# Performance work log

Measured on AMD Instinct MI355X. Metric: run time of the kernel, lower is better.

## Reference

```python
import jax, jax.numpy as jnp
import numpy as np

NUM_Q = 8      # num_quantizers
K = 1024       # codebook_size (num_tokens)
D = 512        # feature dim
B, T = 16, 2000
BETA = 0.25    # commitment weight


def setup_inputs() -> dict:
    key = jax.random.key(0)
    kx, kc = jax.random.split(key)
    x = jax.random.normal(kx, (B, T, D), dtype=jnp.float32)
    # learned codebooks, one per quantizer stage: [NUM_Q, K, D]
    codebooks = jax.random.normal(kc, (NUM_Q, K, D), dtype=jnp.float32)
    return {"x": x, "codebooks": codebooks}


def _vq_stage(residual, codebook):
    """Single VQ layer: nearest-codeword search + straight-through + commitment loss.
    residual: [B, T, D]; codebook: [K, D]."""
    sg = jax.lax.stop_gradient
    # squared L2 distances via ||r||^2 - 2 r.e + ||e||^2  -> [B, T, K]
    r2 = jnp.sum(residual * residual, axis=-1, keepdims=True)          # [B,T,1]
    e2 = jnp.sum(codebook * codebook, axis=-1)                          # [K]
    dots = jnp.einsum('btd,kd->btk', residual, codebook)                # [B,T,K]
    dist = r2 - 2.0 * dots + e2
    indices = jnp.argmin(dist, axis=-1)                                 # [B,T] int
    quantized = codebook[indices]                                       # [B,T,D] gather
    # commitment + codebook loss (VQ-VAE style)
    loss = (BETA * jnp.mean((sg(quantized) - residual) ** 2)
            + jnp.mean((quantized - sg(residual)) ** 2))
    # straight-through estimator
    quantized_st = residual + sg(quantized - residual)
    return quantized_st, indices, loss


def reference(x, codebooks):
    def step(carry, codebook):
        residual, q_out = carry
        q, idx, loss = _vq_stage(residual, codebook)
        residual = residual - jax.lax.stop_gradient(q)
        return (residual, q_out + q), (idx, loss)

    init = (x, jnp.zeros_like(x))
    (_, quantized_out), (all_indices, all_losses) = jax.lax.scan(step, init, codebooks)
    # all_indices: [NUM_Q, B, T]; mean loss across stages
    return quantized_out, all_indices, jnp.mean(all_losses)
```

## Files before the change

### kernel.cpp

```cpp
#include <hip/hip_runtime.h>

#define M_TOK 32000
#define DIM   512
#define KCB   1024
#define NQ    8
#define BM 256
#define NITER 24

typedef _Float16 f16x8 __attribute__((ext_vector_type(8)));
typedef _Float16 f16x4 __attribute__((ext_vector_type(4)));
typedef float f32x4 __attribute__((ext_vector_type(4)));

#define SBAR() __builtin_amdgcn_s_barrier()
#define SFENCE() __builtin_amdgcn_sched_barrier(0)
#define WAIT_VM(N) asm volatile("s_waitcnt vmcnt(" #N ")" ::: "memory")
#define WAIT_LGKM0() asm volatile("s_waitcnt lgkmcnt(0)" ::: "memory")

__device__ __forceinline__ void gload_lds16(const void* g, void* l) {
  __builtin_amdgcn_global_load_lds(
      (const __attribute__((address_space(1))) unsigned int*)g,
      (__attribute__((address_space(3))) unsigned int*)l, 16, 0, 0);
}

__device__ __forceinline__ float wave_reduce_sum(float v) {
#pragma unroll
  for (int off = 32; off > 0; off >>= 1) v += __shfl_xor(v, off, 64);
  return v;
}

__device__ __forceinline__ unsigned int fenc(float f) {
  unsigned int u = __float_as_uint(f);
  return (u & 0x80000000u) ? ~u : (u | 0x80000000u);
}

__device__ __forceinline__ _Float16 hi16(float v) { return (_Float16)v; }
__device__ __forceinline__ _Float16 lo16(float v, _Float16 h) {
  return (_Float16)(v - (float)h);
}

struct Split4 { f16x4 h, l; };
__device__ __forceinline__ Split4 split4(float4 v) {
  Split4 s;
  s.h[0] = hi16(v.x); s.l[0] = lo16(v.x, s.h[0]);
  s.h[1] = hi16(v.y); s.l[1] = lo16(v.y, s.h[1]);
  s.h[2] = hi16(v.z); s.l[2] = lo16(v.z, s.h[2]);
  s.h[3] = hi16(v.w); s.l[3] = lo16(v.w, s.h[3]);
  return s;
}

__global__ __launch_bounds__(256) void rvq_init_kernel(
    const float* __restrict__ x, const float* __restrict__ cb,
    float* __restrict__ e2, float* __restrict__ r2,
    unsigned long long* __restrict__ keys, float* __restrict__ lossCell,
    _Float16* __restrict__ ahi, _Float16* __restrict__ alo) {
  if (blockIdx.x == 0 && threadIdx.x == 0) *lossCell = 0.f;
  for (int i = blockIdx.x * 256 + threadIdx.x; i < M_TOK; i += gridDim.x * 256)
    keys[i] = ~0ull;
  int row = blockIdx.x * 4 + (threadIdx.x >> 6);
  int lane = threadIdx.x & 63;
  if (row < NQ * KCB) {
    const float4* s4 = (const float4*)(cb + (size_t)row * DIM);
    float s = 0.f;
    float4 v = s4[lane];
    s += v.x * v.x + v.y * v.y + v.z * v.z + v.w * v.w;
    v = s4[lane + 64];
    s += v.x * v.x + v.y * v.y + v.z * v.z + v.w * v.w;
    s = wave_reduce_sum(s);
    if (lane == 0) e2[row] = s;
  } else {
    int t = row - NQ * KCB;
    if (t >= M_TOK) return;
    const float4* s4 = (const float4*)(x + (size_t)t * DIM);
    float4 v0 = s4[lane], v1 = s4[lane + 64];
    float s = v0.x * v0.x + v0.y * v0.y + v0.z * v0.z + v0.w * v0.w
            + v1.x * v1.x + v1.y * v1.y + v1.z * v1.z + v1.w * v1.w;
    Split4 s0 = split4(v0), s1 = split4(v1);
    size_t base = (size_t)t * DIM + lane * 4;
    *(f16x4*)(ahi + base) = s0.h;
    *(f16x4*)(alo + base) = s0.l;
    *(f16x4*)(ahi + base + 256) = s1.h;
    *(f16x4*)(alo + base + 256) = s1.l;
    s = wave_reduce_sum(s);
    if (lane == 0) r2[t] = s;
  }
}

__global__ __launch_bounds__(256) void rvq_split_cb_kernel(
    const float* __restrict__ cb, _Float16* __restrict__ cbF) {
  int gid = blockIdx.x * 256 + threadIdx.x;
  int lane = gid & 63;
  int g = (gid >> 6) & 7;
  int half = (gid >> 9) & 1;
  int nc = (gid >> 10) & 3;
  int bt = (gid >> 12) & 31;
  int s = gid >> 17;
  if (s >= NQ) return;
  int col = nc * 256 + half * 128 + (g >> 2) * 64 + (g & 3) * 16 + (lane & 15);
  int ko = (bt & 15) * 32 + (lane >> 4) * 8;
  const float* src = cb + ((size_t)s * KCB + col) * DIM + ko;
  int isLo = bt >> 4;
  f16x8 out;
#pragma unroll
  for (int j = 0; j < 8; ++j) {
    _Float16 h = hi16(src[j]);
    out[j] = isLo ? lo16(src[j], h) : h;
  }
  *(f16x8*)(cbF + (size_t)gid * 8) = out;
}

__global__ __launch_bounds__(512, 2) void rvq_argmin_kernel(
    const _Float16* __restrict__ ahi,
    const _Float16* __restrict__ alo,
    const _Float16* __restrict__ cbFs,
    const float* __restrict__ e2,
    const float* __restrict__ r2,
    unsigned long long* __restrict__ keys) {
  __shared__ _Float16 bufA[2][2][2][4096];
  __shared__ _Float16 bufB[2][2][2][4096];

  const int tid = threadIdx.x;
  const int lane = tid & 63, w = tid >> 6;
  const int l15 = lane & 15, l4 = lane >> 4;
  const int wr = w >> 2, wc = w & 3;

  const int bid = blockIdx.x;
  const int xcd = bid & 7, org = bid >> 3;
  const int wg = ((xcd < 4) ? xcd * 63 : 252 + (xcd - 4) * 62) + org;
  const int m0 = (wg >> 2) * BM;
  const int nc = wg & 3;

  auto stage = [&](int nb, int tIter, int hp) {
    const int ktl = hp >> 2, half = hp & 1, isB = (hp >> 1) & 1;
    const int t = tIter * 2 + ktl;
    const int j = t & 15, p = t >> 4;
    if (!isB) {
      const _Float16* plane = (p == 2) ? alo : ahi;
      const int row = m0 + half * 128 + w * 16 + l15;
      const int ko = j * 32 + l4 * 8;
      gload_lds16(plane + (size_t)row * 512 + ko, &bufA[nb][ktl][half][w * 512]);
    } else {
      const int bt = (p == 1) ? 16 + j : j;
      const _Float16* base = cbFs + (((size_t)(bt * 4 + nc)) * 2 + half) * 4096;
      gload_lds16(base + tid * 8, &bufB[nb][ktl][half][w * 512]);
    }
  };

  f32x4 acc[8][4];
#pragma unroll
  for (int a = 0; a < 8; ++a)
#pragma unroll
    for (int b = 0; b < 4; ++b) acc[a][b] = (f32x4){0.f, 0.f, 0.f, 0.f};

#pragma unroll
  for (int hp = 0; hp < 8; ++hp) stage(0, 0, hp);
  WAIT_VM(4);
  SBAR();

  for (int it = 0; it < NITER; ++it) {
    const int pb = it & 1, nb = pb ^ 1;
    const int nt = (it + 1 == NITER) ? 0 : it + 1;
#pragma unroll
    for (int ph = 0; ph < 4; ++ph) {
      const int kt = ph >> 1, mfh = ph & 1;
      const _Float16* As = &bufA[pb][kt][wr][0];
      const _Float16* Bs = &bufB[pb][kt][wc >> 1][0];
      f16x8 af[4], bf[4];
#pragma unroll
      for (int i = 0; i < 4; ++i)
        af[i] = *(const f16x8*)(As + ((mfh * 4 + i) * 64 + lane) * 8);
#pragma unroll
      for (int i = 0; i < 4; ++i)
        bf[i] = *(const f16x8*)(Bs + (((wc & 1) * 4 + i) * 64 + lane) * 8);
      SFENCE();
      stage(nb, nt, 2 * ph);
      stage(nb, nt, 2 * ph + 1);
      if (ph == 1) WAIT_VM(4);
      if (ph == 3) WAIT_VM(4);
      SBAR();
      WAIT_LGKM0();
      SFENCE();
      __builtin_amdgcn_s_setprio(1);
#pragma unroll
      for (int j = 0; j < 4; ++j)
#pragma unroll
        for (int i = 0; i < 4; ++i)
          acc[mfh * 4 + i][j] = __builtin_amdgcn_mfma_f32_16x16x32_f16(
              af[i], bf[j], acc[mfh * 4 + i][j], 0, 0, 0);
      __builtin_amdgcn_s_setprio(0);
      SBAR();
    }
  }
  WAIT_VM(0);

  const int colbase = nc * 256 + (wc >> 1) * 128 + (wc & 1) * 64;
  float minv[32];
  int mini[32];
#pragma unroll
  for (int i = 0; i < 32; ++i) { minv[i] = 3.4e38f; mini[i] = 0; }
#pragma unroll
  for (int nf = 0; nf < 4; ++nf) {
    float e2v = e2[colbase + nf * 16 + l15];
    int colg = colbase + nf * 16 + l15;
#pragma unroll
    for (int mf = 0; mf < 8; ++mf) {
      float4 rv = *(const float4*)(r2 + m0 + wr * 128 + mf * 16 + l4 * 4);
      float rva[4] = {rv.x, rv.y, rv.z, rv.w};
#pragma unroll
      for (int rr = 0; rr < 4; ++rr) {
        float d = (rva[rr] - 2.f * acc[mf][nf][rr]) + e2v;
        int ii = mf * 4 + rr;
        if (d < minv[ii]) { minv[ii] = d; mini[ii] = colg; }
      }
    }
  }
#pragma unroll
  for (int mf = 0; mf < 8; ++mf) {
#pragma unroll
    for (int rr = 0; rr < 4; ++rr) {
      int ii = mf * 4 + rr;
      float v = minv[ii];
      int ix = mini[ii];
#pragma unroll
      for (int off = 8; off; off >>= 1) {
        float ov = __shfl_xor(v, off, 16);
        int oi = __shfl_xor(ix, off, 16);
        if (ov < v || (ov == v && oi < ix)) { v = ov; ix = oi; }
      }
      if (l15 == 0) {
        int tok = m0 + wr * 128 + mf * 16 + l4 * 4 + rr;
        unsigned long long key = ((unsigned long long)fenc(v) << 32) | (unsigned)ix;
        atomicMin(&keys[tok], key);
      }
    }
  }
}

__global__ __launch_bounds__(256) void rvq_update_kernel(
    const float* __restrict__ rin, const float* __restrict__ cb,
    unsigned long long* __restrict__ keys,
    float* __restrict__ rout, float* __restrict__ r2out,
    float* __restrict__ idx_out, float* __restrict__ lossCell,
    _Float16* __restrict__ ahi, _Float16* __restrict__ alo) {
  const int wave = threadIdx.x >> 6, lane = threadIdx.x & 63;
  __shared__ float lred[4];
  float lpart = 0.f;
  for (int r = wave; r < 64; r += 4) {
    const int tok = blockIdx.x * 64 + r;
    const unsigned idx = (unsigned)(keys[tok] & 0xffffffffu);
    const float4* rrow = (const float4*)(rin + (size_t)tok * DIM);
    const float4* crow = (const float4*)(cb + (size_t)idx * DIM);
    float4* orow = (float4*)(rout + (size_t)tok * DIM);
    float ssq_t = 0.f, ssq_r = 0.f;
#pragma unroll
    for (int c4 = 0; c4 < 2; ++c4) {
      int c = lane + c4 * 64;
      float4 a = rrow[c], q = crow[c];
      float4 t = make_float4(q.x - a.x, q.y - a.y, q.z - a.z, q.w - a.w);
      float4 qst = make_float4(a.x + t.x, a.y + t.y, a.z + t.z, a.w + t.w);
      float4 rn = make_float4(a.x - qst.x, a.y - qst.y, a.z - qst.z, a.w - qst.w);
      orow[c] = rn;
      Split4 sp = split4(rn);
      *(f16x4*)(ahi + (size_t)tok * DIM + c * 4) = sp.h;
      *(f16x4*)(alo + (size_t)tok * DIM + c * 4) = sp.l;
      ssq_t += t.x * t.x + t.y * t.y + t.z * t.z + t.w * t.w;
      ssq_r += rn.x * rn.x + rn.y * rn.y + rn.z * rn.z + rn.w * rn.w;
    }
    float tot_t = wave_reduce_sum(ssq_t);
    float tot_r = wave_reduce_sum(ssq_r);
    if (lane == 0) {
      idx_out[tok] = (float)idx;
      keys[tok] = ~0ull;
      r2out[tok] = tot_r;
      lpart += tot_t;
    }
  }
  if (lane == 0) lred[wave] = lpart;
  __syncthreads();
  if (threadIdx.x == 0)
    atomicAdd(lossCell, lred[0] + lred[1] + lred[2] + lred[3]);
}

__global__ __launch_bounds__(256) void rvq_finalize_kernel(
    const float* __restrict__ x, float* __restrict__ out,
    const float* __restrict__ lossCell, float* __restrict__ loss_out) {
  size_t i = (size_t)blockIdx.x * 256 + threadIdx.x;
  const size_t n4 = (size_t)M_TOK * DIM / 4;
  if (i < n4) {
    const float4* x4 = (const float4*)x;
    float4* o4 = (float4*)out;
    float4 a = x4[i], r = o4[i];
    o4[i] = make_float4(a.x - r.x, a.y - r.y, a.z - r.z, a.w - r.w);
  }
  if (blockIdx.x == 0 && threadIdx.x == 0) {
    *loss_out = *lossCell * (1.25f / 131072000.f);
  }
}

extern "C" void kernel_launch(void* const* d_in, const int* in_sizes, int n_in,
                              void* d_out, int out_size, void* d_ws, size_t ws_size,
                              hipStream_t stream) {
  const float* x = (const float*)d_in[0];
  const float* cb = (const float*)d_in[1];
  float* out = (float*)d_out;
  float* idx_out = out + (size_t)M_TOK * DIM;
  float* loss_out = idx_out + (size_t)NQ * M_TOK;

  char* wsp = (char*)d_ws;
  unsigned long long* keys = (unsigned long long*)wsp;
  float* e2 = (float*)(wsp + 262144);
  float* r2 = (float*)(wsp + 294912);
  float* lossCell = (float*)(wsp + 425984);
  _Float16* cbF = (_Float16*)(wsp + 524288);
  _Float16* ahi = (_Float16*)(wsp + 524288 + 16777216);
  _Float16* alo = ahi + (size_t)M_TOK * DIM;

  {
    int rows = NQ * KCB + M_TOK;
    rvq_init_kernel<<<(rows + 3) / 4, 256, 0, stream>>>(x, cb, e2, r2, keys,
                                                        lossCell, ahi, alo);
    rvq_split_cb_kernel<<<(NQ << 17) / 256, 256, 0, stream>>>(cb, cbF);
  }
  float* resbuf = out;
  const size_t stageF = (size_t)1 << 20;
  for (int s = 0; s < NQ; ++s) {
    const float* rin = (s == 0) ? x : resbuf;
    rvq_argmin_kernel<<<(M_TOK / BM) * 4, 512, 0, stream>>>(
        ahi, alo, cbF + (size_t)s * stageF, e2 + s * KCB, r2, keys);
    rvq_update_kernel<<<M_TOK / 64, 256, 0, stream>>>(
        rin, cb + (size_t)s * KCB * DIM, keys, resbuf, r2,
        idx_out + (size_t)s * M_TOK, lossCell, ahi, alo);
  }
  rvq_finalize_kernel<<<(M_TOK * DIM / 4 + 255) / 256, 256, 0, stream>>>(
      x, out, lossCell, loss_out);
}
```

Baseline: 1.297 ms.

## Switch argmin GEMM to triple-buffered LDS pipeline with one barrier per k-tile

Restructures the main argmin GEMM loop. The old double-buffered, four-phase-per-iteration schedule becomes a triple-buffered ring that prefetches two k-tiles ahead and uses a single barrier per tile. Each wave now loads all 8 A fragments and 4 B fragments per tile and issues 32 MFMAs between barriers, and the codebook pre-split layout is changed to match. LDS usage rises to about 96KB, so launch bounds drop to one block per CU. Fewer barriers and deeper prefetch are traded for lower occupancy.

```diff
diff --git a/kernel.cpp b/kernel.cpp
--- a/kernel.cpp
+++ b/kernel.cpp
@@ -5,7 +5,7 @@
 #define KCB   1024
 #define NQ    8
 #define BM 256
-#define NITER 24
+#define NT 48
 
 typedef _Float16 f16x8 __attribute__((ext_vector_type(8)));
 typedef _Float16 f16x4 __attribute__((ext_vector_type(4)));
@@ -14,7 +14,6 @@
 #define SBAR() __builtin_amdgcn_s_barrier()
 #define SFENCE() __builtin_amdgcn_sched_barrier(0)
 #define WAIT_VM(N) asm volatile("s_waitcnt vmcnt(" #N ")" ::: "memory")
-#define WAIT_LGKM0() asm volatile("s_waitcnt lgkmcnt(0)" ::: "memory")
 
 __device__ __forceinline__ void gload_lds16(const void* g, void* l) {
   __builtin_amdgcn_global_load_lds(
@@ -88,16 +87,14 @@
 __global__ __launch_bounds__(256) void rvq_split_cb_kernel(
     const float* __restrict__ cb, _Float16* __restrict__ cbF) {
   int gid = blockIdx.x * 256 + threadIdx.x;
-  int lane = gid & 63;
-  int g = (gid >> 6) & 7;
-  int half = (gid >> 9) & 1;
+  int c = gid & 1023;
   int nc = (gid >> 10) & 3;
   int bt = (gid >> 12) & 31;
   int s = gid >> 17;
   if (s >= NQ) return;
-  int col = nc * 256 + half * 128 + (g >> 2) * 64 + (g & 3) * 16 + (lane & 15);
-  int ko = (bt & 15) * 32 + (lane >> 4) * 8;
-  const float* src = cb + ((size_t)s * KCB + col) * DIM + ko;
+  int col = nc * 256 + (c >> 6) * 16 + (c & 15);
+  int k = (bt & 15) * 32 + ((c >> 4) & 3) * 8;
+  const float* src = cb + ((size_t)s * KCB + col) * DIM + k;
   int isLo = bt >> 4;
   f16x8 out;
 #pragma unroll
@@ -108,15 +105,15 @@
   *(f16x8*)(cbF + (size_t)gid * 8) = out;
 }
 
-__global__ __launch_bounds__(512, 2) void rvq_argmin_kernel(
+__global__ __launch_bounds__(512, 1) void rvq_argmin_kernel(
     const _Float16* __restrict__ ahi,
     const _Float16* __restrict__ alo,
-    const _Float16* __restrict__ cbFs,
+    const _Float16* __restrict__ cbF,
     const float* __restrict__ e2,
     const float* __restrict__ r2,
     unsigned long long* __restrict__ keys) {
-  __shared__ _Float16 bufA[2][2][2][4096];
-  __shared__ _Float16 bufB[2][2][2][4096];
+  __shared__ _Float16 bufA[3][8192];
+  __shared__ _Float16 bufB[3][8192];
 
   const int tid = threadIdx.x;
   const int lane = tid & 63, w = tid >> 6;
@@ -129,21 +126,23 @@
   const int m0 = (wg >> 2) * BM;
   const int nc = wg & 3;
 
-  auto stage = [&](int nb, int tIter, int hp) {
-    const int ktl = hp >> 2, half = hp & 1, isB = (hp >> 1) & 1;
-    const int t = tIter * 2 + ktl;
-    const int j = t & 15, p = t >> 4;
-    if (!isB) {
-      const _Float16* plane = (p == 2) ? alo : ahi;
-      const int row = m0 + half * 128 + w * 16 + l15;
-      const int ko = j * 32 + l4 * 8;
-      gload_lds16(plane + (size_t)row * 512 + ko, &bufA[nb][ktl][half][w * 512]);
-    } else {
-      const int bt = (p == 1) ? 16 + j : j;
-      const _Float16* base = cbFs + (((size_t)(bt * 4 + nc)) * 2 + half) * 4096;
-      gload_lds16(base + tid * 8, &bufB[nb][ktl][half][w * 512]);
-    }
+  const int c0 = tid, c1 = tid + 512;
+  const size_t aoff0 = (size_t)(m0 + (c0 >> 6) * 16 + (c0 & 15)) * DIM + ((c0 >> 4) & 3) * 8;
+  const size_t aoff1 = (size_t)(m0 + (c1 >> 6) * 16 + (c1 & 15)) * DIM + ((c1 >> 4) & 3) * 8;
+
+  auto stageB = [&](int t, _Float16* dst) {
+    int j = t & 15;
+    int bt = (t >= 16 && t < 32) ? 16 + j : j;
+    const _Float16* src = cbF + (size_t)(bt * 4 + nc) * 8192;
+    gload_lds16(src + (size_t)c0 * 8, dst + (size_t)c0 * 8);
+    gload_lds16(src + (size_t)c1 * 8, dst + (size_t)c1 * 8);
   };
+  auto stageA = [&](int t, _Float16* dst) {
+    const _Float16* plane = (t >= 32) ? alo : ahi;
+    const int ko = (t & 15) * 32;
+    gload_lds16(plane + aoff0 + ko, dst + (size_t)c0 * 8);
+    gload_lds16(plane + aoff1 + ko, dst + (size_t)c1 * 8);
+  };
 
   f32x4 acc[8][4];
 #pragma unroll
@@ -151,56 +150,54 @@
 #pragma unroll
     for (int b = 0; b < 4; ++b) acc[a][b] = (f32x4){0.f, 0.f, 0.f, 0.f};
 
-#pragma unroll
-  for (int hp = 0; hp < 8; ++hp) stage(0, 0, hp);
+  stageB(0, bufB[0]); stageA(0, bufA[0]);
+  stageB(1, bufB[1]); stageA(1, bufA[1]);
   WAIT_VM(4);
+  SFENCE();
   SBAR();
-
-  for (int it = 0; it < NITER; ++it) {
-    const int pb = it & 1, nb = pb ^ 1;
-    const int nt = (it + 1 == NITER) ? 0 : it + 1;
-#pragma unroll
-    for (int ph = 0; ph < 4; ++ph) {
-      const int kt = ph >> 1, mfh = ph & 1;
-      const _Float16* As = &bufA[pb][kt][wr][0];
-      const _Float16* Bs = &bufB[pb][kt][wc >> 1][0];
-      f16x8 af[4], bf[4];
-#pragma unroll
-      for (int i = 0; i < 4; ++i)
-        af[i] = *(const f16x8*)(As + ((mfh * 4 + i) * 64 + lane) * 8);
-#pragma unroll
-      for (int i = 0; i < 4; ++i)
-        bf[i] = *(const f16x8*)(Bs + (((wc & 1) * 4 + i) * 64 + lane) * 8);
-      SFENCE();
-      stage(nb, nt, 2 * ph);
-      stage(nb, nt, 2 * ph + 1);
-      if (ph == 1) WAIT_VM(4);
-      if (ph == 3) WAIT_VM(4);
-      SBAR();
-      WAIT_LGKM0();
+  SFENCE();
+
+  for (int it6 = 0; it6 < NT; it6 += 6) {
+#pragma unroll
+    for (int ph = 0; ph < 6; ++ph) {
+      const int t = it6 + ph;
+      const int rb = ph % 3;
+      const int wb = (ph + 2) % 3;
+      if (t < NT - 2) { stageB(t + 2, bufB[wb]); stageA(t + 2, bufA[wb]); }
+      const _Float16* As = bufA[rb];
+      const _Float16* Bs = bufB[rb];
+      f16x8 af[8], bf[4];
+#pragma unroll
+      for (int mf = 0; mf < 8; ++mf)
+        af[mf] = *(const f16x8*)(As + ((size_t)(wr * 8 + mf) * 64 + lane) * 8);
+#pragma unroll
+      for (int nf = 0; nf < 4; ++nf)
+        bf[nf] = *(const f16x8*)(Bs + ((size_t)(wc * 4 + nf) * 64 + lane) * 8);
+      if (t < NT - 2) { WAIT_VM(4); } else { WAIT_VM(0); }
       SFENCE();
       __builtin_amdgcn_s_setprio(1);
 #pragma unroll
-      for (int j = 0; j < 4; ++j)
-#pragma unroll
-        for (int i = 0; i < 4; ++i)
-          acc[mfh * 4 + i][j] = __builtin_amdgcn_mfma_f32_16x16x32_f16(
-              af[i], bf[j], acc[mfh * 4 + i][j], 0, 0, 0);
+      for (int nf = 0; nf < 4; ++nf)
+#pragma unroll
+        for (int mf = 0; mf < 8; ++mf)
+          acc[mf][nf] = __builtin_amdgcn_mfma_f32_16x16x32_f16(
+              af[mf], bf[nf], acc[mf][nf], 0, 0, 0);
       __builtin_amdgcn_s_setprio(0);
+      SFENCE();
       SBAR();
-    }
-  }
-  WAIT_VM(0);
-
-  const int colbase = nc * 256 + (wc >> 1) * 128 + (wc & 1) * 64;
+      SFENCE();
+    }
+  }
+
+  const int colbase = nc * 256 + wc * 64;
   float minv[32];
   int mini[32];
 #pragma unroll
   for (int i = 0; i < 32; ++i) { minv[i] = 3.4e38f; mini[i] = 0; }
 #pragma unroll
   for (int nf = 0; nf < 4; ++nf) {
-    float e2v = e2[colbase + nf * 16 + l15];
     int colg = colbase + nf * 16 + l15;
+    float e2v = e2[colg];
 #pragma unroll
     for (int mf = 0; mf < 8; ++mf) {
       float4 rv = *(const float4*)(r2 + m0 + wr * 128 + mf * 16 + l4 * 4);
```

Result: faster. 1.267 ms (-2.3%).
